# Optimization experiments

Measured on AMD Instinct MI355X. Metric: run time of the kernel, lower is better.

## Reference

```python
import jax, jax.numpy as jnp
import numpy as np

N, E, CIN, COUT, KHOP = 100000, 600000, 128, 128, 3


def setup_inputs() -> dict:
    key = jax.random.key(0)
    k1, k2, k3 = jax.random.split(key, 3)
    x = jax.random.normal(k1, (N, CIN), dtype=jnp.float32)
    edge_index = jax.random.randint(k2, (2, E), 0, N, dtype=jnp.int64)
    # xavier_uniform init for weight [in, out]
    limit = float(np.sqrt(6.0 / (CIN + COUT)))
    weight = jax.random.uniform(k3, (CIN, COUT), minval=-limit, maxval=limit, dtype=jnp.float32)
    bias = jnp.zeros((COUT,), jnp.float32)
    log_scale = jnp.asarray(np.log(1.0), jnp.float32)  # init_scale = 1.0
    hop_logits = jnp.zeros((KHOP + 1,), jnp.float32)
    return {"x": x, "edge_index": edge_index, "num_nodes": N,
            "weight": weight, "bias": bias,
            "log_scale": log_scale, "hop_logits": hop_logits}


def reference(x, edge_index, num_nodes, weight, bias, log_scale, hop_logits):
    src, dst = edge_index[0], edge_index[1]
    # symmetric normalization D_src^{-1/2} A D_dst^{-1/2}, no self-loops
    ones = jnp.ones(src.shape, x.dtype)
    deg_src = jax.ops.segment_sum(ones, src, num_segments=num_nodes)
    deg_dst = jax.ops.segment_sum(ones, dst, num_segments=num_nodes)
    dsi = jnp.where(deg_src > 0, jax.lax.rsqrt(jnp.maximum(deg_src, 1.0)), 0.0)
    ddi = jnp.where(deg_dst > 0, jax.lax.rsqrt(jnp.maximum(deg_dst, 1.0)), 0.0)
    edge_weight = dsi[src] * ddi[dst]  # [E]

    s = jnp.exp(log_scale)
    alpha = jax.nn.softmax(hop_logits)  # [k_hop+1]

    wavelet_out = alpha[0] * x
    current = x
    for k in range(1, KHOP + 1):  # small fixed hop count
        # A_hat @ current : gather -> scale -> scatter-add
        current = jax.ops.segment_sum(current[src] * edge_weight[:, None], dst,
                                      num_segments=num_nodes)
        decay = jnp.exp(-s * k)
        wavelet_out = wavelet_out + alpha[k] * decay * current

    return wavelet_out @ weight + bias
```

## Files before the change

### kernel.cpp

```cpp
#include <hip/hip_runtime.h>
#include <hip/hip_bf16.h>

#define C 128

typedef short s16x8 __attribute__((ext_vector_type(8)));
typedef float f32x4 __attribute__((ext_vector_type(4)));

static __device__ __forceinline__ float b2f(unsigned short u) {
    union { unsigned int i; float f; } v;
    v.i = ((unsigned int)u) << 16;
    return v.f;
}
static __device__ __forceinline__ unsigned short f2b(float f) {
    __hip_bfloat16 b = __float2bfloat16(f);
    return *reinterpret_cast<unsigned short*>(&b);
}

__global__ __launch_bounds__(256) void zero_int_kernel(int* __restrict__ p, long n) {
    long i = blockIdx.x * 256L + threadIdx.x;
    if (i < n) p[i] = 0;
}

__global__ __launch_bounds__(256) void hist_kernel(
    const int* __restrict__ ei, int E,
    int* __restrict__ degs, int* __restrict__ degd) {
    int e = blockIdx.x * 256 + threadIdx.x;
    if (e < E) {
        atomicAdd(&degs[ei[e]], 1);
        atomicAdd(&degd[ei[E + e]], 1);
    }
}

__global__ __launch_bounds__(256) void wt_kernel(const float* __restrict__ W,
                                                 unsigned short* __restrict__ WtB,
                                                 const float* __restrict__ log_scale,
                                                 const float* __restrict__ hop_logits,
                                                 float* __restrict__ coef) {
    int tid = blockIdx.x * 256 + threadIdx.x;
    int k = tid & 127, c = tid >> 7;
    WtB[c * 128 + k] = f2b(W[k * 128 + c]);
    if (tid == 0) {
        float s = expf(log_scale[0]);
        float m = hop_logits[0];
        for (int kk = 1; kk < 4; ++kk) m = fmaxf(m, hop_logits[kk]);
        float a[4], sum = 0.0f;
        for (int kk = 0; kk < 4; ++kk) { a[kk] = expf(hop_logits[kk] - m); sum += a[kk]; }
        for (int kk = 0; kk < 4; ++kk) coef[kk] = (a[kk] / sum) * expf(-s * (float)kk);
    }
}

__global__ __launch_bounds__(256) void scan1_kernel(const int* __restrict__ degd,
                                                    int* __restrict__ rp,
                                                    int* __restrict__ bsum, int N) {
    __shared__ int sm[256];
    int t = threadIdx.x;
    int i = blockIdx.x * 256 + t;
    int v = (i < N) ? degd[i] : 0;
    sm[t] = v;
    __syncthreads();
    for (int off = 1; off < 256; off <<= 1) {
        int add = (t >= off) ? sm[t - off] : 0;
        __syncthreads();
        sm[t] += add;
        __syncthreads();
    }
    if (i < N) rp[i] = sm[t] - v;
    if (t == 255) bsum[blockIdx.x] = sm[255];
}

__global__ __launch_bounds__(512) void scan2_kernel(int* __restrict__ bsum, int nb) {
    __shared__ int sm[512];
    int t = threadIdx.x;
    int v = (t < nb) ? bsum[t] : 0;
    sm[t] = v;
    __syncthreads();
    for (int off = 1; off < 512; off <<= 1) {
        int add = (t >= off) ? sm[t - off] : 0;
        __syncthreads();
        sm[t] += add;
        __syncthreads();
    }
    if (t < nb) bsum[t] = sm[t] - v;
}

__global__ __launch_bounds__(256) void scan3_kernel(int* __restrict__ rp,
                                                    const int* __restrict__ bsum,
                                                    int* __restrict__ cursor,
                                                    const int* __restrict__ degs,
                                                    const int* __restrict__ degd,
                                                    float* __restrict__ dsi,
                                                    float* __restrict__ ddi,
                                                    int N, int E) {
    int i = blockIdx.x * 256 + threadIdx.x;
    if (i < N) {
        int v = rp[i] + bsum[i >> 8];
        rp[i] = v;
        cursor[i] = v;
        int ds = degs[i];
        dsi[i] = ds > 0 ? rsqrtf((float)ds) : 0.0f;
        int dd = degd[i];
        ddi[i] = dd > 0 ? rsqrtf((float)dd) : 0.0f;
    }
    if (i == 0) rp[N] = E;
}

__global__ __launch_bounds__(256) void scatter_kernel(const int* __restrict__ ei, int E,
                                                      int* __restrict__ cursor,
                                                      const float* __restrict__ dsi,
                                                      int2* __restrict__ csr) {
    int e = blockIdx.x * 256 + threadIdx.x;
    if (e < E) {
        int s = ei[e];
        int d = ei[E + e];
        int pos = atomicAdd(&cursor[d], 1);
        csr[pos] = make_int2(s, __float_as_int(dsi[s]));
    }
}

template<int SRCF32>
__global__ __launch_bounds__(256) void pull_kernel(
    const int* __restrict__ rp, const int2* __restrict__ csr,
    const float* __restrict__ ddi,
    const void* __restrict__ cur, unsigned int* __restrict__ nxt, int N) {
    int wid = (int)((blockIdx.x * 256L + threadIdx.x) >> 6);
    if (wid >= N) return;
    int lane = threadIdx.x & 63;
    int beg = __builtin_amdgcn_readfirstlane(rp[wid]);
    int end = __builtin_amdgcn_readfirstlane(rp[wid + 1]);
    const float2* curf = (const float2*)cur;
    const unsigned int* curb = (const unsigned int*)cur;
    float sx = 0.f, sy = 0.f;
    if (beg < end) {
        for (int j = beg; j < end; j += 8) {
            int   idx[8];
            float wt[8];
            #pragma unroll
            for (int i = 0; i < 8; ++i) {
                int jj = j + i;
                bool ok = jj < end;
                int2 e = csr[ok ? jj : beg];
                idx[i] = e.x;
                wt[i] = ok ? __int_as_float(e.y) : 0.0f;
            }
            if (SRCF32) {
                float2 v[8];
                #pragma unroll
                for (int i = 0; i < 8; ++i) v[i] = curf[(long)idx[i] * 64 + lane];
                #pragma unroll
                for (int i = 0; i < 8; ++i) { sx += wt[i] * v[i].x; sy += wt[i] * v[i].y; }
            } else {
                unsigned int u[8];
                #pragma unroll
                for (int i = 0; i < 8; ++i) u[i] = curb[(long)idx[i] * 64 + lane];
                #pragma unroll
                for (int i = 0; i < 8; ++i) {
                    sx += wt[i] * b2f((unsigned short)(u[i] & 0xffff));
                    sy += wt[i] * b2f((unsigned short)(u[i] >> 16));
                }
            }
        }
        float dv = ddi[wid];
        sx *= dv; sy *= dv;
    }
    unsigned int o = (unsigned int)f2b(sx) | ((unsigned int)f2b(sy) << 16);
    nxt[(long)wid * 64 + lane] = o;
}

__global__ __launch_bounds__(256) void mfma_matmul_kernel(
    const float* __restrict__ x,
    const unsigned short* __restrict__ h1,
    const unsigned short* __restrict__ h2,
    const unsigned short* __restrict__ h3,
    const float* __restrict__ coef,
    const unsigned short* __restrict__ WtB,
    const float* __restrict__ bias,
    float* __restrict__ out, int N) {
    __shared__ unsigned short Wl[128 * 136];
    int t = threadIdx.x;

    #pragma unroll
    for (int i = 0; i < 8; ++i) {
        int ch = t + i * 256;
        int r = ch >> 4;
        int ko = (ch & 15) * 8;
        *(s16x8*)(Wl + r * 136 + ko) = *(const s16x8*)(WtB + r * 128 + ko);
    }
    float c0 = coef[0], c1 = coef[1], c2 = coef[2], c3 = coef[3];
    __syncthreads();

    int wave = t >> 6, lane = t & 63;
    int lsel = lane & 15;
    int lk   = (lane >> 4) * 8;
    int arow = blockIdx.x * 64 + wave * 16 + lsel;
    bool rok = arow < N;
    long rbase = (long)arow * C;

    f32x4 acc[8];
    #pragma unroll
    for (int i = 0; i < 8; ++i) acc[i] = (f32x4){0.f, 0.f, 0.f, 0.f};

    #pragma unroll
    for (int ks = 0; ks < 4; ++ks) {
        int k0 = ks * 32 + lk;
        s16x8 a;
        if (rok) {
            const float* xp = x + rbase + k0;
            float4 xa = *(const float4*)xp;
            float4 xb = *(const float4*)(xp + 4);
            s16x8 u1 = *(const s16x8*)(h1 + rbase + k0);
            s16x8 u2 = *(const s16x8*)(h2 + rbase + k0);
            s16x8 u3 = *(const s16x8*)(h3 + rbase + k0);
            float f0 = c0 * xa.x + c1 * b2f((unsigned short)u1[0]) + c2 * b2f((unsigned short)u2[0]) + c3 * b2f((unsigned short)u3[0]);
            float f1 = c0 * xa.y + c1 * b2f((unsigned short)u1[1]) + c2 * b2f((unsigned short)u2[1]) + c3 * b2f((unsigned short)u3[1]);
            float f2 = c0 * xa.z + c1 * b2f((unsigned short)u1[2]) + c2 * b2f((unsigned short)u2[2]) + c3 * b2f((unsigned short)u3[2]);
            float f3 = c0 * xa.w + c1 * b2f((unsigned short)u1[3]) + c2 * b2f((unsigned short)u2[3]) + c3 * b2f((unsigned short)u3[3]);
            float f4 = c0 * xb.x + c1 * b2f((unsigned short)u1[4]) + c2 * b2f((unsigned short)u2[4]) + c3 * b2f((unsigned short)u3[4]);
            float f5 = c0 * xb.y + c1 * b2f((unsigned short)u1[5]) + c2 * b2f((unsigned short)u2[5]) + c3 * b2f((unsigned short)u3[5]);
            float f6 = c0 * xb.z + c1 * b2f((unsigned short)u1[6]) + c2 * b2f((unsigned short)u2[6]) + c3 * b2f((unsigned short)u3[6]);
            float f7 = c0 * xb.w + c1 * b2f((unsigned short)u1[7]) + c2 * b2f((unsigned short)u2[7]) + c3 * b2f((unsigned short)u3[7]);
            a[0] = (short)f2b(f0); a[1] = (short)f2b(f1);
            a[2] = (short)f2b(f2); a[3] = (short)f2b(f3);
            a[4] = (short)f2b(f4); a[5] = (short)f2b(f5);
            a[6] = (short)f2b(f6); a[7] = (short)f2b(f7);
        } else {
            a = (s16x8)0;
        }
        #pragma unroll
        for (int cf = 0; cf < 8; ++cf) {
            s16x8 b = *(const s16x8*)(Wl + (cf * 16 + lsel) * 136 + k0);
            acc[cf] = __builtin_amdgcn_mfma_f32_16x16x32_bf16(a, b, acc[cf], 0, 0, 0);
        }
    }

    int orow0 = blockIdx.x * 64 + wave * 16 + (lane >> 4) * 4;
    #pragma unroll
    for (int cf = 0; cf < 8; ++cf) {
        int ocol = cf * 16 + lsel;
        float bv = bias[ocol];
        #pragma unroll
        for (int r = 0; r < 4; ++r) {
            int orow = orow0 + r;
            if (orow < N) out[(long)orow * C + ocol] = acc[cf][r] + bv;
        }
    }
}

extern "C" void kernel_launch(void* const* d_in, const int* in_sizes, int n_in,
                              void* d_out, int out_size, void* d_ws, size_t ws_size,
                              hipStream_t stream) {
    const float* x          = (const float*)d_in[0];
    const int*   ei         = (const int*)d_in[1];
    const float* W          = (const float*)d_in[3];
    const float* bias       = (const float*)d_in[4];
    const float* log_scale  = (const float*)d_in[5];
    const float* hop_logits = (const float*)d_in[6];
    float* out = (float*)d_out;

    int N = in_sizes[0] / C;
    int E = in_sizes[1] / 2;

    char* ws = (char*)d_ws;
    size_t hb = (size_t)N * C * sizeof(unsigned short);
    unsigned short* h1 = (unsigned short*)ws;
    unsigned short* h2 = (unsigned short*)(ws + hb);
    unsigned short* h3 = (unsigned short*)(ws + 2 * hb);
    int2*  csr     = (int2*)(ws + 3 * hb);
    int*   degs    = (int*)(csr + E);
    int*   degd    = degs + N;
    int*   rp      = degd + N;
    int*   cursor  = rp + N + 1;
    float* dsi     = (float*)(cursor + N);
    float* ddi     = dsi + N;
    int*   bsum    = (int*)(ddi + N);
    float* coef    = (float*)(bsum + 512);
    unsigned short* WtB = (unsigned short*)(coef + 4);

    int eb  = (E + 255) / 256;
    int nbk = (N + 255) / 256;
    int pull_blocks = (int)(((long)N * 64 + 255) / 256);

    zero_int_kernel<<<(int)((2L * N + 255) / 256), 256, 0, stream>>>(degs, 2L * N);
    hist_kernel<<<eb, 256, 0, stream>>>(ei, E, degs, degd);
    wt_kernel<<<64, 256, 0, stream>>>(W, WtB, log_scale, hop_logits, coef);
    scan1_kernel<<<nbk, 256, 0, stream>>>(degd, rp, bsum, N);
    scan2_kernel<<<1, 512, 0, stream>>>(bsum, nbk);
    scan3_kernel<<<nbk, 256, 0, stream>>>(rp, bsum, cursor, degs, degd, dsi, ddi, N, E);
    scatter_kernel<<<eb, 256, 0, stream>>>(ei, E, cursor, dsi, csr);

    pull_kernel<1><<<pull_blocks, 256, 0, stream>>>(rp, csr, ddi, x,  (unsigned int*)h1, N);
    pull_kernel<0><<<pull_blocks, 256, 0, stream>>>(rp, csr, ddi, h1, (unsigned int*)h2, N);
    pull_kernel<0><<<pull_blocks, 256, 0, stream>>>(rp, csr, ddi, h2, (unsigned int*)h3, N);

    mfma_matmul_kernel<<<(N + 63) / 64, 256, 0, stream>>>(x, h1, h2, h3, coef, WtB, bias, out, N);
}
```

Baseline: 249.0 us.

## Fuse third propagation hop with combine-and-matmul; vectorize edge-preprocessing kernels

The third gather/scatter hop is merged into the final matmul kernel. Each 512-thread block pulls 8 rows, combines them with x, h1 and h2 into bf16 rows in LDS, and runs a 16x16 MFMA tile against W read straight from global memory. This drops the h3 buffer and its write and re-read, plus one launch. The trade is that half of each MFMA tile is zero padding and W fragments are reloaded per block instead of staged in LDS. The histogram, scatter and zero kernels now handle 4 edges or ints per thread with int4 loads.

Result: slower. 273.8 us (+10.0%).

```diff
diff --git a/kernel.cpp b/kernel.cpp
--- a/kernel.cpp
+++ b/kernel.cpp
@@ -16,18 +16,28 @@
     return *reinterpret_cast<unsigned short*>(&b);
 }
 
-__global__ __launch_bounds__(256) void zero_int_kernel(int* __restrict__ p, long n) {
+__global__ __launch_bounds__(256) void zero_int_kernel(int4* __restrict__ p, long n4) {
     long i = blockIdx.x * 256L + threadIdx.x;
-    if (i < n) p[i] = 0;
+    if (i < n4) p[i] = make_int4(0, 0, 0, 0);
 }
 
 __global__ __launch_bounds__(256) void hist_kernel(
     const int* __restrict__ ei, int E,
     int* __restrict__ degs, int* __restrict__ degd) {
-    int e = blockIdx.x * 256 + threadIdx.x;
-    if (e < E) {
-        atomicAdd(&degs[ei[e]], 1);
-        atomicAdd(&degd[ei[E + e]], 1);
+    int i = blockIdx.x * 256 + threadIdx.x;
+    int e0 = i * 4;
+    if (e0 + 4 <= E) {
+        int4 s = *(const int4*)(ei + e0);
+        int4 d = *(const int4*)(ei + E + e0);
+        atomicAdd(&degs[s.x], 1); atomicAdd(&degs[s.y], 1);
+        atomicAdd(&degs[s.z], 1); atomicAdd(&degs[s.w], 1);
+        atomicAdd(&degd[d.x], 1); atomicAdd(&degd[d.y], 1);
+        atomicAdd(&degd[d.z], 1); atomicAdd(&degd[d.w], 1);
+    } else {
+        for (int e = e0; e < E; ++e) {
+            atomicAdd(&degs[ei[e]], 1);
+            atomicAdd(&degd[ei[E + e]], 1);
+        }
     }
 }
 
@@ -108,12 +118,26 @@
                                                       int* __restrict__ cursor,
                                                       const float* __restrict__ dsi,
                                                       int2* __restrict__ csr) {
-    int e = blockIdx.x * 256 + threadIdx.x;
-    if (e < E) {
-        int s = ei[e];
-        int d = ei[E + e];
-        int pos = atomicAdd(&cursor[d], 1);
-        csr[pos] = make_int2(s, __float_as_int(dsi[s]));
+    int i = blockIdx.x * 256 + threadIdx.x;
+    int e0 = i * 4;
+    if (e0 + 4 <= E) {
+        int4 s = *(const int4*)(ei + e0);
+        int4 d = *(const int4*)(ei + E + e0);
+        int p0 = atomicAdd(&cursor[d.x], 1);
+        int p1 = atomicAdd(&cursor[d.y], 1);
+        int p2 = atomicAdd(&cursor[d.z], 1);
+        int p3 = atomicAdd(&cursor[d.w], 1);
+        csr[p0] = make_int2(s.x, __float_as_int(dsi[s.x]));
+        csr[p1] = make_int2(s.y, __float_as_int(dsi[s.y]));
+        csr[p2] = make_int2(s.z, __float_as_int(dsi[s.z]));
+        csr[p3] = make_int2(s.w, __float_as_int(dsi[s.w]));
+    } else {
+        for (int e = e0; e < E; ++e) {
+            int s = ei[e];
+            int d = ei[E + e];
+            int pos = atomicAdd(&cursor[d], 1);
+            csr[pos] = make_int2(s, __float_as_int(dsi[s]));
+        }
     }
 }
 
@@ -166,81 +190,87 @@
     nxt[(long)wid * 64 + lane] = o;
 }
 
-__global__ __launch_bounds__(256) void mfma_matmul_kernel(
+__global__ __launch_bounds__(512, 6) void pull3_mm_kernel(
+    const int* __restrict__ rp, const int2* __restrict__ csr,
+    const float* __restrict__ ddi,
     const float* __restrict__ x,
     const unsigned short* __restrict__ h1,
     const unsigned short* __restrict__ h2,
-    const unsigned short* __restrict__ h3,
     const float* __restrict__ coef,
     const unsigned short* __restrict__ WtB,
     const float* __restrict__ bias,
     float* __restrict__ out, int N) {
-    __shared__ unsigned short Wl[128 * 136];
+    __shared__ unsigned short Xl[16 * 136];
     int t = threadIdx.x;
-
-    #pragma unroll
-    for (int i = 0; i < 8; ++i) {
-        int ch = t + i * 256;
-        int r = ch >> 4;
-        int ko = (ch & 15) * 8;
-        *(s16x8*)(Wl + r * 136 + ko) = *(const s16x8*)(WtB + r * 128 + ko);
-    }
+    int w = t >> 6, lane = t & 63;
+    int wid = blockIdx.x * 8 + w;
     float c0 = coef[0], c1 = coef[1], c2 = coef[2], c3 = coef[3];
+
+    float sx = 0.f, sy = 0.f;
+    if (wid < N) {
+        int beg = __builtin_amdgcn_readfirstlane(rp[wid]);
+        int end = __builtin_amdgcn_readfirstlane(rp[wid + 1]);
+        const unsigned int* curb = (const unsigned int*)h2;
+        if (beg < end) {
+            for (int j = beg; j < end; j += 8) {
+                int   idx[8];
+                float wt[8];
+                #pragma unroll
+                for (int i = 0; i < 8; ++i) {
+                    int jj = j + i;
+                    bool ok = jj < end;
+                    int2 e = csr[ok ? jj : beg];
+                    idx[i] = e.x;
+                    wt[i] = ok ? __int_as_float(e.y) : 0.0f;
+                }
+                unsigned int u[8];
+                #pragma unroll
+                for (int i = 0; i < 8; ++i) u[i] = curb[(long)idx[i] * 64 + lane];
+                #pragma unroll
+                for (int i = 0; i < 8; ++i) {
+                    sx += wt[i] * b2f((unsigned short)(u[i] & 0xffff));
+                    sy += wt[i] * b2f((unsigned short)(u[i] >> 16));
+                }
+            }
+            float dv = ddi[wid];
+            sx *= dv; sy *= dv;
+        }
+        long rbase = (long)wid * C;
+        float2 xv = ((const float2*)(x + rbase))[lane];
+        unsigned int u1 = ((const unsigned int*)(h1 + rbase))[lane];
+        unsigned int u2 = ((const unsigned int*)(h2 + rbase))[lane];
+        float f0 = c0 * xv.x + c1 * b2f((unsigned short)(u1 & 0xffff))
+                 + c2 * b2f((unsigned short)(u2 & 0xffff)) + c3 * sx;
+        float f1 = c0 * xv.y + c1 * b2f((unsigned short)(u1 >> 16))
+                 + c2 * b2f((unsigned short)(u2 >> 16)) + c3 * sy;
+        sx = f0; sy = f1;
+    } else {
+        sx = 0.f; sy = 0.f;
+    }
+    unsigned int pk = (unsigned int)f2b(sx) | ((unsigned int)f2b(sy) << 16);
+    *(unsigned int*)(Xl + w * 136 + lane * 2) = pk;
+    *(unsigned int*)(Xl + (w + 8) * 136 + lane * 2) = 0u;
     __syncthreads();
 
-    int wave = t >> 6, lane = t & 63;
     int lsel = lane & 15;
-    int lk   = (lane >> 4) * 8;
-    int arow = blockIdx.x * 64 + wave * 16 + lsel;
-    bool rok = arow < N;
-    long rbase = (long)arow * C;
-
-    f32x4 acc[8];
-    #pragma unroll
-    for (int i = 0; i < 8; ++i) acc[i] = (f32x4){0.f, 0.f, 0.f, 0.f};
-
+    int lk = (lane >> 4) * 8;
+    f32x4 acc = (f32x4){0.f, 0.f, 0.f, 0.f};
     #pragma unroll
     for (int ks = 0; ks < 4; ++ks) {
         int k0 = ks * 32 + lk;
-        s16x8 a;
-        if (rok) {
-            const float* xp = x + rbase + k0;
-            float4 xa = *(const float4*)xp;
-            float4 xb = *(const float4*)(xp + 4);
-            s16x8 u1 = *(const s16x8*)(h1 + rbase + k0);
-            s16x8 u2 = *(const s16x8*)(h2 + rbase + k0);
-            s16x8 u3 = *(const s16x8*)(h3 + rbase + k0);
-            float f0 = c0 * xa.x + c1 * b2f((unsigned short)u1[0]) + c2 * b2f((unsigned short)u2[0]) + c3 * b2f((unsigned short)u3[0]);
-            float f1 = c0 * xa.y + c1 * b2f((unsigned short)u1[1]) + c2 * b2f((unsigned short)u2[1]) + c3 * b2f((unsigned short)u3[1]);
-            float f2 = c0 * xa.z + c1 * b2f((unsigned short)u1[2]) + c2 * b2f((unsigned short)u2[2]) + c3 * b2f((unsigned short)u3[2]);
-            float f3 = c0 * xa.w + c1 * b2f((unsigned short)u1[3]) + c2 * b2f((unsigned short)u2[3]) + c3 * b2f((unsigned short)u3[3]);
-            float f4 = c0 * xb.x + c1 * b2f((unsigned short)u1[4]) + c2 * b2f((unsigned short)u2[4]) + c3 * b2f((unsigned short)u3[4]);
-            float f5 = c0 * xb.y + c1 * b2f((unsigned short)u1[5]) + c2 * b2f((unsigned short)u2[5]) + c3 * b2f((unsigned short)u3[5]);
-            float f6 = c0 * xb.z + c1 * b2f((unsigned short)u1[6]) + c2 * b2f((unsigned short)u2[6]) + c3 * b2f((unsigned short)u3[6]);
-            float f7 = c0 * xb.w + c1 * b2f((unsigned short)u1[7]) + c2 * b2f((unsigned short)u2[7]) + c3 * b2f((unsigned short)u3[7]);
-            a[0] = (short)f2b(f0); a[1] = (short)f2b(f1);
-            a[2] = (short)f2b(f2); a[3] = (short)f2b(f3);
-            a[4] = (short)f2b(f4); a[5] = (short)f2b(f5);
-            a[6] = (short)f2b(f6); a[7] = (short)f2b(f7);
-        } else {
-            a = (s16x8)0;
-        }
-        #pragma unroll
-        for (int cf = 0; cf < 8; ++cf) {
-            s16x8 b = *(const s16x8*)(Wl + (cf * 16 + lsel) * 136 + k0);
-            acc[cf] = __builtin_amdgcn_mfma_f32_16x16x32_bf16(a, b, acc[cf], 0, 0, 0);
-        }
-    }
-
-    int orow0 = blockIdx.x * 64 + wave * 16 + (lane >> 4) * 4;
+        s16x8 a = *(const s16x8*)(Xl + lsel * 136 + k0);
+        s16x8 b = *(const s16x8*)(WtB + (w * 16 + lsel) * 128 + k0);
+        acc = __builtin_amdgcn_mfma_f32_16x16x32_bf16(a, b, acc, 0, 0, 0);
+    }
+    int r0 = (lane >> 4) * 4;
+    int ocol = w * 16 + lsel;
+    float bv = bias[ocol];
     #pragma unroll
-    for (int cf = 0; cf < 8; ++cf) {
-        int ocol = cf * 16 + lsel;
-        float bv = bias[ocol];
-        #pragma unroll
-        for (int r = 0; r < 4; ++r) {
-            int orow = orow0 + r;
-            if (orow < N) out[(long)orow * C + ocol] = acc[cf][r] + bv;
+    for (int r = 0; r < 4; ++r) {
+        int row = r0 + r;
+        if (row < 8) {
+            int orow = blockIdx.x * 8 + row;
+            if (orow < N) out[(long)orow * C + ocol] = acc[r] + bv;
         }
     }
 }
@@ -263,8 +293,7 @@
     size_t hb = (size_t)N * C * sizeof(unsigned short);
     unsigned short* h1 = (unsigned short*)ws;
     unsigned short* h2 = (unsigned short*)(ws + hb);
-    unsigned short* h3 = (unsigned short*)(ws + 2 * hb);
-    int2*  csr     = (int2*)(ws + 3 * hb);
+    int2*  csr     = (int2*)(ws + 2 * hb);
     int*   degs    = (int*)(csr + E);
     int*   degd    = degs + N;
     int*   rp      = degd + N;
@@ -275,21 +304,21 @@
     float* coef    = (float*)(bsum + 512);
     unsigned short* WtB = (unsigned short*)(coef + 4);
 
-    int eb  = (E + 255) / 256;
+    int eb4 = (E / 4 + 255) / 256 + 1;
     int nbk = (N + 255) / 256;
     int pull_blocks = (int)(((long)N * 64 + 255) / 256);
 
-    zero_int_kernel<<<(int)((2L * N + 255) / 256), 256, 0, stream>>>(degs, 2L * N);
-    hist_kernel<<<eb, 256, 0, stream>>>(ei, E, degs, degd);
+    zero_int_kernel<<<(int)((2L * N / 4 + 255) / 256), 256, 0, stream>>>((int4*)degs, 2L * N / 4);
+    hist_kernel<<<eb4, 256, 0, stream>>>(ei, E, degs, degd);
     wt_kernel<<<64, 256, 0, stream>>>(W, WtB, log_scale, hop_logits, coef);
     scan1_kernel<<<nbk, 256, 0, stream>>>(degd, rp, bsum, N);
     scan2_kernel<<<1, 512, 0, stream>>>(bsum, nbk);
     scan3_kernel<<<nbk, 256, 0, stream>>>(rp, bsum, cursor, degs, degd, dsi, ddi, N, E);
-    scatter_kernel<<<eb, 256, 0, stream>>>(ei, E, cursor, dsi, csr);
+    scatter_kernel<<<eb4, 256, 0, stream>>>(ei, E, cursor, dsi, csr);
 
     pull_kernel<1><<<pull_blocks, 256, 0, stream>>>(rp, csr, ddi, x,  (unsigned int*)h1, N);
     pull_kernel<0><<<pull_blocks, 256, 0, stream>>>(rp, csr, ddi, h1, (unsigned int*)h2, N);
-    pull_kernel<0><<<pull_blocks, 256, 0, stream>>>(rp, csr, ddi, h2, (unsigned int*)h3, N);
-
-    mfma_matmul_kernel<<<(N + 63) / 64, 256, 0, stream>>>(x, h1, h2, h3, coef, WtB, bias, out, N);
-}
+
+    pull3_mm_kernel<<<(N + 7) / 8, 512, 0, stream>>>(rp, csr, ddi, x, h1, h2,
+                                                     coef, WtB, bias, out, N);
+}
```
